# Performance work log

Hardware: AMD Instinct MI355X
Metric: run time of the kernel (lower is better)

## Reference

```python
import jax, jax.numpy as jnp
import numpy as np

N = 100000
E = 1600000
DIM_IN, DIM_H, DIM_OUT = 48, 48, 48


def gcn_conv(x, edge_index, W, b):
    # PyG GCNConv: add self-loops, symmetric normalization D^-1/2 (A+I) D^-1/2, linear first.
    n = x.shape[0]
    loop = jnp.arange(n, dtype=edge_index.dtype)
    row = jnp.concatenate([edge_index[0], loop])  # sources
    col = jnp.concatenate([edge_index[1], loop])  # targets
    deg = jax.ops.segment_sum(jnp.ones_like(col, dtype=x.dtype), col, num_segments=n)
    dinv = jnp.where(deg > 0, jax.lax.rsqrt(jnp.maximum(deg, 1e-12)), 0.0)
    norm = dinv[row] * dinv[col]  # [E+N]
    h = x @ W  # [N, out]
    msg = h[row] * norm[:, None]  # gather + scale, [E+N, out]
    out = jax.ops.segment_sum(msg, col, num_segments=n)  # scatter-add
    return out + b


def setup_inputs() -> dict:
    key = jax.random.key(0)
    ks = jax.random.split(key, 8)
    x = jax.random.normal(ks[0], (N, DIM_IN), dtype=jnp.float32)
    edge_index = jax.random.randint(ks[1], (2, E), 0, N, dtype=jnp.int64)
    s1 = 1.0 / np.sqrt(DIM_IN)
    s2 = 1.0 / np.sqrt(DIM_H)
    s3 = 1.0 / np.sqrt(DIM_OUT)
    W1 = jax.random.uniform(ks[2], (DIM_IN, DIM_H), jnp.float32, -s1, s1)
    b1 = jnp.zeros((DIM_H,), jnp.float32)
    W2 = jax.random.uniform(ks[3], (DIM_H, DIM_OUT), jnp.float32, -s2, s2)
    b2 = jnp.zeros((DIM_OUT,), jnp.float32)
    Wlin = jax.random.uniform(ks[4], (DIM_OUT, 2), jnp.float32, -s3, s3)
    blin = jax.random.uniform(ks[5], (2,), jnp.float32, -s3, s3)
    return {"x": x, "edge_index": edge_index, "W1": W1, "b1": b1, "W2": W2, "b2": b2, "Wlin": Wlin, "blin": blin}


def reference(x, edge_index, W1, b1, W2, b2, Wlin, blin):
    h = gcn_conv(x, edge_index, W1, b1)
    h = jax.nn.leaky_relu(h, negative_slope=0.01)
    h = gcn_conv(h, edge_index, W2, b2)
    # global_add_pool with all-zero batch ids -> sum over all nodes, [1, DIM_OUT]
    g = jnp.sum(h, axis=0, keepdims=True)
    # dropout is identity in eval mode
    return g @ Wlin + blin  # [1, 2]
```

## Files before the change

kernel.cpp:

```cpp
#include <hip/hip_runtime.h>
#include <hip/hip_bf16.h>
#include <hip/hip_fp8.h>

#define DIM 48
#define HS8 64
#define BKN 256
#define BSH 8
#define CAP 5248
#define NB1MAX 400
#define EPT 6
#define GNPB 64
#define GTPN 3

typedef float v2f __attribute__((ext_vector_type(2)));

__device__ inline unsigned pack_fp8x4(float a, float b, float c, float d) {
#if __has_builtin(__builtin_amdgcn_cvt_pk_fp8_f32)
    int w = __builtin_amdgcn_cvt_pk_fp8_f32(a, b, 0, false);
    w = __builtin_amdgcn_cvt_pk_fp8_f32(c, d, w, true);
    return (unsigned)w;
#else
    __hip_fp8_e4m3 qa(a), qb(b), qc(c), qd(d);
    return (unsigned)qa.__x | ((unsigned)qb.__x << 8) |
           ((unsigned)qc.__x << 16) | ((unsigned)qd.__x << 24);
#endif
}

__device__ inline void acc_fp8x4(unsigned w, float* acc) {
#if __has_builtin(__builtin_amdgcn_cvt_pk_f32_fp8)
    v2f lo = __builtin_amdgcn_cvt_pk_f32_fp8((int)w, false);
    v2f hi = __builtin_amdgcn_cvt_pk_f32_fp8((int)w, true);
    acc[0] += lo[0]; acc[1] += lo[1]; acc[2] += hi[0]; acc[3] += hi[1];
#else
    __hip_fp8_e4m3 q0, q1, q2, q3;
    q0.__x = (unsigned char)(w & 0xff);
    q1.__x = (unsigned char)((w >> 8) & 0xff);
    q2.__x = (unsigned char)((w >> 16) & 0xff);
    q3.__x = (unsigned char)(w >> 24);
    acc[0] += (float)q0; acc[1] += (float)q1;
    acc[2] += (float)q2; acc[3] += (float)q3;
#endif
}

__device__ inline void acc_fp8x16(uint4 v, float* acc) {
    acc_fp8x4(v.x, acc + 0);
    acc_fp8x4(v.y, acc + 4);
    acc_fp8x4(v.z, acc + 8);
    acc_fp8x4(v.w, acc + 12);
}

__global__ void k_zero(int* __restrict__ cntc, int* __restrict__ cntr,
                       float* __restrict__ g, int nb1) {
    int i = blockIdx.x * blockDim.x + threadIdx.x;
    if (i < nb1) { cntc[i] = 0; cntr[i] = 0; }
    if (i < 64) g[i] = 0.0f;
}

__global__ __launch_bounds__(512) void k_part(
    const int* __restrict__ row, const int* __restrict__ col,
    int* __restrict__ cntc, int* __restrict__ cntr,
    unsigned* __restrict__ partc, unsigned* __restrict__ partr, int E, int nb1) {
    __shared__ int hc[NB1MAX], hr[NB1MAX];
    __shared__ int bc_[NB1MAX], br_[NB1MAX];
    int t = threadIdx.x;
    int lo = blockIdx.x * (512 * EPT);
    int hi = min(lo + 512 * EPT, E);
    int ec[EPT], er[EPT];
    int m = 0;
    for (int e = lo + t; e < hi; e += 512) { ec[m] = col[e]; er[m] = row[e]; ++m; }
    for (int i = t; i < nb1; i += 512) { hc[i] = 0; hr[i] = 0; }
    __syncthreads();
    for (int k = 0; k < m; ++k) {
        atomicAdd(&hc[ec[k] >> BSH], 1);
        atomicAdd(&hr[er[k] >> BSH], 1);
    }
    __syncthreads();
    for (int i = t; i < nb1; i += 512) {
        bc_[i] = hc[i] ? atomicAdd(&cntc[i], hc[i]) : 0;
        br_[i] = hr[i] ? atomicAdd(&cntr[i], hr[i]) : 0;
        hc[i] = 0; hr[i] = 0;
    }
    __syncthreads();
    for (int k = 0; k < m; ++k) {
        int c = ec[k], r = er[k];
        int b1 = c >> BSH;
        unsigned p1 = (unsigned)(bc_[b1] + atomicAdd(&hc[b1], 1));
        if (p1 < (unsigned)CAP)
            partc[(size_t)b1 * CAP + p1] = ((unsigned)(c & (BKN - 1)) << 24) | (unsigned)r;
        int b2 = r >> BSH;
        unsigned p2 = (unsigned)(br_[b2] + atomicAdd(&hr[b2], 1));
        if (p2 < (unsigned)CAP)
            partr[(size_t)b2 * CAP + p2] = ((unsigned)(r & (BKN - 1)) << 24) | (unsigned)c;
    }
}

__global__ __launch_bounds__(512) void k_sortp(
    const unsigned* __restrict__ partc, const int* __restrict__ cntc,
    int* __restrict__ nodpk, float* __restrict__ dinv,
    int* __restrict__ srcs, int N, int nb1) {
    __shared__ int cnt[BKN];
    __shared__ int cur[BKN];
    __shared__ int sc[BKN];
    __shared__ int outb[CAP];
    int b = blockIdx.x, t = threadIdx.x;
    int nlo = b << BSH;
    int nE = min(cntc[b], CAP);
    const unsigned* pp = partc + (size_t)b * CAP;
    if (t < BKN) cnt[t] = 0;
    __syncthreads();
    for (int e = t; e < nE; e += 512)
        atomicAdd(&cnt[pp[e] >> 24], 1);
    __syncthreads();
    int v = 0;
    if (t < BKN) { v = cnt[t]; sc[t] = v; }
    __syncthreads();
    for (int off = 1; off < BKN; off <<= 1) {
        int u = 0;
        if (t < BKN && t >= off) u = sc[t - off];
        __syncthreads();
        if (t < BKN) sc[t] += u;
        __syncthreads();
    }
    if (t < BKN) {
        int ex = (t == 0) ? 0 : sc[t - 1];
        if (nlo + t < N) {
            nodpk[nlo + t] = ex | (v << 16);
            dinv[nlo + t] = 1.0f / sqrtf((float)(v + 1));
        }
        cur[t] = ex;
    }
    __syncthreads();
    for (int e = t; e < nE; e += 512) {
        unsigned p = pp[e];
        int s = atomicAdd(&cur[p >> 24], 1);
        outb[s] = (int)(p & 0xffffffu);
    }
    __syncthreads();
    int* sb = srcs + (size_t)b * CAP;
    for (int i2 = t; i2 < nE; i2 += 512) sb[i2] = outb[i2];
}

__global__ __launch_bounds__(512) void k_wsum(
    const unsigned* __restrict__ partr, const int* __restrict__ cntr,
    const float* __restrict__ dinv, float* __restrict__ wfin, int N, int nb1) {
    __shared__ float ws[BKN];
    int b = blockIdx.x, t = threadIdx.x;
    if (t < BKN) ws[t] = 0.0f;
    __syncthreads();
    int nE = min(cntr[b], CAP);
    const unsigned* pp = partr + (size_t)b * CAP;
    for (int e = t; e < nE; e += 512) {
        unsigned p = pp[e];
        atomicAdd(&ws[p >> 24], dinv[p & 0xffffffu]);
    }
    __syncthreads();
    int j = (b << BSH) + t;
    if (t < BKN && j < N) {
        float dj = dinv[j];
        wfin[j] = (ws[t] + dj) * dj;
    }
}

__global__ void k_mm_scale(const float* __restrict__ in, const float* __restrict__ W,
                           const float* __restrict__ dinv,
                           unsigned char* __restrict__ hs8, int n) {
    __shared__ float Ws[DIM * DIM];
    for (int i = threadIdx.x; i < DIM * DIM; i += blockDim.x) Ws[i] = W[i];
    __syncthreads();
    int node = blockIdx.x * blockDim.x + threadIdx.x;
    if (node >= n) return;
    float xr[DIM];
    const float4* xp = (const float4*)(in + (size_t)node * DIM);
    #pragma unroll
    for (int j = 0; j < DIM / 4; ++j) {
        float4 v = xp[j];
        xr[j * 4 + 0] = v.x; xr[j * 4 + 1] = v.y;
        xr[j * 4 + 2] = v.z; xr[j * 4 + 3] = v.w;
    }
    float o[DIM];
    #pragma unroll
    for (int f = 0; f < DIM; ++f) o[f] = 0.0f;
    for (int k = 0; k < DIM; ++k) {
        float xv = xr[k];
        #pragma unroll
        for (int f = 0; f < DIM; ++f) o[f] = fmaf(xv, Ws[k * DIM + f], o[f]);
    }
    float d = dinv[node];
    uint4* hp = (uint4*)(hs8 + (size_t)node * HS8);
    #pragma unroll
    for (int q = 0; q < 3; ++q) {
        uint4 v;
        v.x = pack_fp8x4(o[q*16+ 0]*d, o[q*16+ 1]*d, o[q*16+ 2]*d, o[q*16+ 3]*d);
        v.y = pack_fp8x4(o[q*16+ 4]*d, o[q*16+ 5]*d, o[q*16+ 6]*d, o[q*16+ 7]*d);
        v.z = pack_fp8x4(o[q*16+ 8]*d, o[q*16+ 9]*d, o[q*16+10]*d, o[q*16+11]*d);
        v.w = pack_fp8x4(o[q*16+12]*d, o[q*16+13]*d, o[q*16+14]*d, o[q*16+15]*d);
        hp[q] = v;
    }
}

__global__ __launch_bounds__(GNPB * GTPN) void k_gather1f(
    const unsigned char* __restrict__ hs8,
    const int* __restrict__ nodpk, const int* __restrict__ srcs,
    const float* __restrict__ dinv, const float* __restrict__ wfin,
    const float* __restrict__ bias, float* __restrict__ g, int n) {
    __shared__ float gsum[DIM];
    int t = threadIdx.x;
    if (t < DIM) gsum[t] = 0.0f;
    __syncthreads();
    int local = t / GTPN;
    int c = t - local * GTPN;
    int i = blockIdx.x * GNPB + local;
    bool valid = (i < n);
    float ov[16];
    if (valid) {
        int pk = nodpk[i];
        int start = (i >> BSH) * CAP + (pk & 0xffff);
        int end = start + (pk >> 16);
        float d = dinv[i];
        float w = wfin[i];
        const unsigned char* hb = hs8 + (size_t)c * 16;
        float acc[16];
        #pragma unroll
        for (int k = 0; k < 16; ++k) acc[k] = 0.0f;
        uint4 sv = *(const uint4*)(hb + (size_t)i * HS8);
        acc_fp8x16(sv, acc);
        for (int j = start; j < end; ++j) {
            uint4 v = *(const uint4*)(hb + (size_t)srcs[j] * HS8);
            acc_fp8x16(v, acc);
        }
        #pragma unroll
        for (int k = 0; k < 16; ++k) {
            float vv = acc[k] * d + bias[c * 16 + k];
            vv = (vv >= 0.0f) ? vv : 0.01f * vv;
            ov[k] = vv * w;
        }
    }
    if (valid) {
        #pragma unroll
        for (int k = 0; k < 16; ++k) atomicAdd(&gsum[c * 16 + k], ov[k]);
    }
    __syncthreads();
    if (t < DIM) atomicAdd(&g[t], gsum[t]);
}

__global__ void k_final2(const float* __restrict__ g, const float* __restrict__ W2,
                         const float* __restrict__ b2, const float* __restrict__ Wlin,
                         const float* __restrict__ blin, float* __restrict__ out, int n) {
    __shared__ float gp[DIM];
    int t = threadIdx.x;
    if (t < DIM) {
        float s = (float)n * b2[t];
        for (int q = 0; q < DIM; ++q) s += g[q] * W2[q * DIM + t];
        gp[t] = s;
    }
    __syncthreads();
    if (t < 2) {
        float s = blin[t];
        for (int f = 0; f < DIM; ++f) s += gp[f] * Wlin[f * 2 + t];
        out[t] = s;
    }
}

static inline char* alignup(char* p, size_t a) {
    return (char*)(((uintptr_t)p + a - 1) & ~(uintptr_t)(a - 1));
}

extern "C" void kernel_launch(void* const* d_in, const int* in_sizes, int n_in,
                              void* d_out, int out_size, void* d_ws, size_t ws_size,
                              hipStream_t stream) {
    const float* x    = (const float*)d_in[0];
    const int*   ei   = (const int*)d_in[1];
    const float* W1   = (const float*)d_in[2];
    const float* b1   = (const float*)d_in[3];
    const float* W2   = (const float*)d_in[4];
    const float* b2   = (const float*)d_in[5];
    const float* Wlin = (const float*)d_in[6];
    const float* blin = (const float*)d_in[7];
    float* out = (float*)d_out;

    int N = in_sizes[0] / DIM;
    int E = in_sizes[1] / 2;
    const int* row = ei;
    const int* col = ei + E;
    int nb1 = (N + BKN - 1) / BKN;

    char* p = (char*)d_ws;
    int* cntc = (int*)p;                  p = alignup(p + nb1 * 4, 64);
    int* cntr = (int*)p;                  p = alignup(p + nb1 * 4, 64);
    int* nodpk = (int*)p;                 p = alignup(p + (size_t)N * 4, 64);
    float* dinv = (float*)p;              p = alignup(p + (size_t)N * 4, 64);
    float* wfin = (float*)p;              p = alignup(p + (size_t)N * 4, 64);
    float* g = (float*)p;                 p = alignup(p + 64 * 4, 64);
    unsigned* partc = (unsigned*)p;       p = alignup(p + (size_t)nb1 * CAP * 4, 64);
    unsigned* partr = (unsigned*)p;       p = alignup(p + (size_t)nb1 * CAP * 4, 64);
    int* srcs = (int*)p;                  p = alignup(p + (size_t)nb1 * CAP * 4, 64);
    unsigned char* hs8 = (unsigned char*)p;

    int nblk = (N + 255) / 256;
    int gblk = (N + GNPB - 1) / GNPB;
    int pblk = (E + 512 * EPT - 1) / (512 * EPT);

    k_zero<<<(nb1 + 255) / 256, 256, 0, stream>>>(cntc, cntr, g, nb1);
    k_part<<<pblk, 512, 0, stream>>>(row, col, cntc, cntr, partc, partr, E, nb1);
    k_sortp<<<nb1, 512, 0, stream>>>(partc, cntc, nodpk, dinv, srcs, N, nb1);
    k_wsum<<<nb1, 512, 0, stream>>>(partr, cntr, dinv, wfin, N, nb1);

    k_mm_scale<<<nblk, 256, 0, stream>>>(x, W1, dinv, hs8, N);
    k_gather1f<<<gblk, GNPB * GTPN, 0, stream>>>(hs8, nodpk, srcs, dinv, wfin, b1, g, N);

    k_final2<<<1, 64, 0, stream>>>(g, W2, b2, Wlin, blin, out, N);
}
```

Baseline: 149.3 us.

## Compact CSR source list with global block offsets and pack dinv/weight into float2

Adds a one-block scan kernel over the per-bucket edge counts so the sorted source indices are stored contiguously (size E) instead of in padded CAP-strided buckets. Node offsets now carry a 24-bit global start and 8-bit degree. The separate dinv and wfin arrays are merged into one float2 array so the gather and matmul kernels load both values with a single access. The sort kernel also gains a dummy pass over partr that atomically adds zero into an unused shared array, which is extra work with no effect. Degrees above 255 would be clamped in the packed field.

```diff
diff --git a/kernel.cpp b/kernel.cpp
--- a/kernel.cpp
+++ b/kernel.cpp
@@ -94,25 +94,44 @@
     }
 }
 
-__global__ __launch_bounds__(512) void k_sortp(
+__global__ void k_scanb(const int* __restrict__ cntc, int* __restrict__ bstart, int nb1) {
+    __shared__ int sm[512];
+    int t = threadIdx.x;
+    sm[t] = (t < nb1) ? min(cntc[t], CAP) : 0;
+    __syncthreads();
+    for (int off = 1; off < 512; off <<= 1) {
+        int v = (t >= off) ? sm[t - off] : 0;
+        __syncthreads();
+        sm[t] += v;
+        __syncthreads();
+    }
+    if (t < nb1) bstart[t] = (t == 0) ? 0 : sm[t - 1];
+}
+
+__global__ __launch_bounds__(512) void k_sortw(
     const unsigned* __restrict__ partc, const int* __restrict__ cntc,
-    int* __restrict__ nodpk, float* __restrict__ dinv,
+    const unsigned* __restrict__ partr, const int* __restrict__ cntr,
+    const int* __restrict__ bstart,
+    int* __restrict__ nodpk, float2* __restrict__ wd,
     int* __restrict__ srcs, int N, int nb1) {
     __shared__ int cnt[BKN];
     __shared__ int cur[BKN];
     __shared__ int sc[BKN];
+    __shared__ float ws[BKN];
+    __shared__ float dv[BKN];
     __shared__ int outb[CAP];
     int b = blockIdx.x, t = threadIdx.x;
     int nlo = b << BSH;
     int nE = min(cntc[b], CAP);
+    int gbase = bstart[b];
     const unsigned* pp = partc + (size_t)b * CAP;
-    if (t < BKN) cnt[t] = 0;
+    if (t < BKN) { cnt[t] = 0; ws[t] = 0.0f; }
     __syncthreads();
     for (int e = t; e < nE; e += 512)
         atomicAdd(&cnt[pp[e] >> 24], 1);
     __syncthreads();
     int v = 0;
-    if (t < BKN) { v = cnt[t]; sc[t] = v; }
+    if (t < BKN) { v = min(cnt[t], 255); sc[t] = cnt[t]; }
     __syncthreads();
     for (int off = 1; off < BKN; off <<= 1) {
         int u = 0;
@@ -123,10 +142,9 @@
     }
     if (t < BKN) {
         int ex = (t == 0) ? 0 : sc[t - 1];
-        if (nlo + t < N) {
-            nodpk[nlo + t] = ex | (v << 16);
-            dinv[nlo + t] = 1.0f / sqrtf((float)(v + 1));
-        }
+        float d = 1.0f / sqrtf((float)(cnt[t] + 1));
+        dv[t] = d;
+        if (nlo + t < N) nodpk[nlo + t] = (gbase + ex) | (v << 24);
         cur[t] = ex;
     }
     __syncthreads();
@@ -135,14 +153,22 @@
         int s = atomicAdd(&cur[p >> 24], 1);
         outb[s] = (int)(p & 0xffffffu);
     }
-    __syncthreads();
-    int* sb = srcs + (size_t)b * CAP;
+    int nEr = min(cntr[b], CAP);
+    const unsigned* pr = partr + (size_t)b * CAP;
+    __syncthreads();
+    for (int e = t; e < nEr; e += 512) {
+        unsigned p = pr[e];
+        atomicAdd(&ws[p >> 24], __int_as_float(0));
+    }
+    __syncthreads();
+    int* sb = srcs + gbase;
     for (int i2 = t; i2 < nE; i2 += 512) sb[i2] = outb[i2];
+    if (t < BKN && nlo + t < N) wd[nlo + t] = make_float2(dv[t], 0.0f);
 }
 
 __global__ __launch_bounds__(512) void k_wsum(
     const unsigned* __restrict__ partr, const int* __restrict__ cntr,
-    const float* __restrict__ dinv, float* __restrict__ wfin, int N, int nb1) {
+    float2* __restrict__ wd, int N, int nb1) {
     __shared__ float ws[BKN];
     int b = blockIdx.x, t = threadIdx.x;
     if (t < BKN) ws[t] = 0.0f;
@@ -151,18 +177,18 @@
     const unsigned* pp = partr + (size_t)b * CAP;
     for (int e = t; e < nE; e += 512) {
         unsigned p = pp[e];
-        atomicAdd(&ws[p >> 24], dinv[p & 0xffffffu]);
+        atomicAdd(&ws[p >> 24], wd[p & 0xffffffu].x);
     }
     __syncthreads();
     int j = (b << BSH) + t;
     if (t < BKN && j < N) {
-        float dj = dinv[j];
-        wfin[j] = (ws[t] + dj) * dj;
+        float dj = wd[j].x;
+        wd[j].y = (ws[t] + dj) * dj;
     }
 }
 
 __global__ void k_mm_scale(const float* __restrict__ in, const float* __restrict__ W,
-                           const float* __restrict__ dinv,
+                           const float2* __restrict__ wd,
                            unsigned char* __restrict__ hs8, int n) {
     __shared__ float Ws[DIM * DIM];
     for (int i = threadIdx.x; i < DIM * DIM; i += blockDim.x) Ws[i] = W[i];
@@ -185,7 +211,7 @@
         #pragma unroll
         for (int f = 0; f < DIM; ++f) o[f] = fmaf(xv, Ws[k * DIM + f], o[f]);
     }
-    float d = dinv[node];
+    float d = wd[node].x;
     uint4* hp = (uint4*)(hs8 + (size_t)node * HS8);
     #pragma unroll
     for (int q = 0; q < 3; ++q) {
@@ -201,7 +227,7 @@
 __global__ __launch_bounds__(GNPB * GTPN) void k_gather1f(
     const unsigned char* __restrict__ hs8,
     const int* __restrict__ nodpk, const int* __restrict__ srcs,
-    const float* __restrict__ dinv, const float* __restrict__ wfin,
+    const float2* __restrict__ wd,
     const float* __restrict__ bias, float* __restrict__ g, int n) {
     __shared__ float gsum[DIM];
     int t = threadIdx.x;
@@ -214,10 +240,9 @@
     float ov[16];
     if (valid) {
         int pk = nodpk[i];
-        int start = (i >> BSH) * CAP + (pk & 0xffff);
-        int end = start + (pk >> 16);
-        float d = dinv[i];
-        float w = wfin[i];
+        int start = pk & 0xffffff;
+        int end = start + ((unsigned)pk >> 24);
+        float2 dw = wd[i];
         const unsigned char* hb = hs8 + (size_t)c * 16;
         float acc[16];
         #pragma unroll
@@ -230,9 +255,9 @@
         }
         #pragma unroll
         for (int k = 0; k < 16; ++k) {
-            float vv = acc[k] * d + bias[c * 16 + k];
+            float vv = acc[k] * dw.x + bias[c * 16 + k];
             vv = (vv >= 0.0f) ? vv : 0.01f * vv;
-            ov[k] = vv * w;
+            ov[k] = vv * dw.y;
         }
     }
     if (valid) {
@@ -287,13 +312,13 @@
     char* p = (char*)d_ws;
     int* cntc = (int*)p;                  p = alignup(p + nb1 * 4, 64);
     int* cntr = (int*)p;                  p = alignup(p + nb1 * 4, 64);
+    int* bstart = (int*)p;                p = alignup(p + (nb1 + 1) * 4, 64);
     int* nodpk = (int*)p;                 p = alignup(p + (size_t)N * 4, 64);
-    float* dinv = (float*)p;              p = alignup(p + (size_t)N * 4, 64);
-    float* wfin = (float*)p;              p = alignup(p + (size_t)N * 4, 64);
+    float2* wd = (float2*)p;              p = alignup(p + (size_t)N * 8, 64);
     float* g = (float*)p;                 p = alignup(p + 64 * 4, 64);
     unsigned* partc = (unsigned*)p;       p = alignup(p + (size_t)nb1 * CAP * 4, 64);
     unsigned* partr = (unsigned*)p;       p = alignup(p + (size_t)nb1 * CAP * 4, 64);
-    int* srcs = (int*)p;                  p = alignup(p + (size_t)nb1 * CAP * 4, 64);
+    int* srcs = (int*)p;                  p = alignup(p + (size_t)E * 4, 64);
     unsigned char* hs8 = (unsigned char*)p;
 
     int nblk = (N + 255) / 256;
@@ -302,11 +327,12 @@
 
     k_zero<<<(nb1 + 255) / 256, 256, 0, stream>>>(cntc, cntr, g, nb1);
     k_part<<<pblk, 512, 0, stream>>>(row, col, cntc, cntr, partc, partr, E, nb1);
-    k_sortp<<<nb1, 512, 0, stream>>>(partc, cntc, nodpk, dinv, srcs, N, nb1);
-    k_wsum<<<nb1, 512, 0, stream>>>(partr, cntr, dinv, wfin, N, nb1);
-
-    k_mm_scale<<<nblk, 256, 0, stream>>>(x, W1, dinv, hs8, N);
-    k_gather1f<<<gblk, GNPB * GTPN, 0, stream>>>(hs8, nodpk, srcs, dinv, wfin, b1, g, N);
+    k_scanb<<<1, 512, 0, stream>>>(cntc, bstart, nb1);
+    k_sortw<<<nb1, 512, 0, stream>>>(partc, cntc, partr, cntr, bstart, nodpk, wd, srcs, N, nb1);
+    k_wsum<<<nb1, 512, 0, stream>>>(partr, cntr, wd, N, nb1);
+
+    k_mm_scale<<<nblk, 256, 0, stream>>>(x, W1, wd, hs8, N);
+    k_gather1f<<<gblk, GNPB * GTPN, 0, stream>>>(hs8, nodpk, srcs, wd, b1, g, N);
 
     k_final2<<<1, 64, 0, stream>>>(g, W2, b2, Wlin, blin, out, N);
 }
```

Result: slower. 164.0 us (+9.8%).
